# Performance work log

Measured on AMD Instinct MI355X. Metric: run time of the kernel, lower is better.

Reference implementation:

```python
import jax, jax.numpy as jnp
import numpy as np

RADIUS = 4  # matches init radius


def _bilinear_sample(v, grid):
    """Faithful F.grid_sample(v, grid, mode='bilinear', align_corners=True, padding_mode='zeros').
    v: (B,C,H,W); grid: (B,Hg,Wg,2) in [-1,1]; grid[...,0]->width(x), grid[...,1]->height(y)."""
    B, C, H, W = v.shape
    Hg, Wg = grid.shape[1], grid.shape[2]
    ix = (grid[..., 0] + 1.0) * 0.5 * (W - 1)
    iy = (grid[..., 1] + 1.0) * 0.5 * (H - 1)
    x0 = jnp.floor(ix); y0 = jnp.floor(iy)
    x1 = x0 + 1.0;      y1 = y0 + 1.0
    wx1 = ix - x0; wx0 = 1.0 - wx1
    wy1 = iy - y0; wy0 = 1.0 - wy1
    v_flat = v.reshape(B, C, H * W)
    out = jnp.zeros((B, C, Hg, Wg), v.dtype)
    for xf, yf, w in ((x0, y0, wx0 * wy0), (x1, y0, wx1 * wy0),
                      (x0, y1, wx0 * wy1), (x1, y1, wx1 * wy1)):
        valid = (xf >= 0) & (xf <= W - 1) & (yf >= 0) & (yf <= H - 1)
        xi = jnp.clip(xf, 0, W - 1).astype(jnp.int32)
        yi = jnp.clip(yf, 0, H - 1).astype(jnp.int32)
        idx = (yi * W + xi).reshape(B, 1, Hg * Wg)
        g = jnp.take_along_axis(v_flat, idx, axis=2).reshape(B, C, Hg, Wg)
        out = out + g * (w * valid)[:, None, :, :]
    return out


def setup_inputs() -> dict:
    key = jax.random.key(0)
    ks = jax.random.split(key, 5)
    B, C, H, W, K = 4, 128, 128, 128, 8
    x = jax.random.normal(ks[0], (B, C, H, W), jnp.float32)
    psf_tbl = jax.random.randint(ks[1], (B, H, W, K, 2), 0, 128)  # absolute pixel anchors
    delta = jax.random.normal(ks[2], (1, 1, 1, K, 2), jnp.float32) * 0.1
    w_qkv = jax.random.normal(ks[3], (3 * C, C), jnp.float32) * (C ** -0.5)  # 1x1 conv, no bias
    w_proj = jax.random.normal(ks[4], (C, C), jnp.float32) * (C ** -0.5)
    return {"x": x, "psf_tbl": psf_tbl, "delta": delta, "w_qkv": w_qkv, "w_proj": w_proj}


def reference(x, psf_tbl, delta, w_qkv, w_proj):
    B, C, H, W = x.shape
    K = psf_tbl.shape[3]
    qkv = jnp.einsum('oc,bchw->bohw', w_qkv, x)  # 1x1 conv to_qkv
    q, k, v = jnp.split(qkv, 3, axis=1)
    offsets = psf_tbl.astype(x.dtype) + jnp.tanh(delta) * RADIUS  # (B,H,W,K,2)
    norm = jnp.array([H - 1, W - 1], x.dtype)
    grid = (offsets / norm * 2.0 - 1.0).reshape(B, H, W * K, 2)
    k_s = _bilinear_sample(k, grid).reshape(B, C, H, W, K)
    v_s = _bilinear_sample(v, grid).reshape(B, C, H, W, K)
    attn = jnp.einsum('bchw,bchwk->bhwk', q, k_s) * (C ** -0.5)
    attn = jax.nn.softmax(attn, axis=-1)  # softmax over K sampled points
    out = jnp.einsum('bhwk,bchwk->bchw', attn, v_s)
    return x + jnp.einsum('oc,bchw->bohw', w_proj, out)
```

## Files before the change

kernel.cpp:

```cpp
#include <hip/hip_runtime.h>

#define HW 16384
#define C 128

typedef __attribute__((ext_vector_type(8))) short short8;
typedef __attribute__((ext_vector_type(4))) float f32x4;
typedef __attribute__((ext_vector_type(2))) float f32x2;

__device__ __forceinline__ unsigned short f2bf(float f) {
  union { float f; unsigned u; } v; v.f = f;
  return (unsigned short)((v.u + 0x7fffu + ((v.u >> 16) & 1u)) >> 16);
}
#if __has_builtin(__builtin_amdgcn_cvt_pk_bf16_f32)
typedef __attribute__((ext_vector_type(2))) __bf16 bf16x2;
__device__ __forceinline__ unsigned pk2(float a, float b) {
  union { bf16x2 v; unsigned u; } cv;
  cv.v = __builtin_amdgcn_cvt_pk_bf16_f32(a, b);
  return cv.u;
}
#else
__device__ __forceinline__ unsigned pk2(float a, float b) {
  return (unsigned)f2bf(a) | ((unsigned)f2bf(b) << 16);
}
#endif
__device__ __forceinline__ unsigned short f2bf1(float a) {
  return (unsigned short)(pk2(a, a) & 0xffffu);
}
__device__ __forceinline__ float bflo(unsigned w) {
  union { unsigned u; float f; } v; v.u = w << 16; return v.f;
}
__device__ __forceinline__ float bfhi(unsigned w) {
  union { unsigned u; float f; } v; v.u = w & 0xffff0000u; return v.f;
}
__device__ __forceinline__ float asf(unsigned u) {
  union { unsigned u; float f; } v; v.u = u; return v.f;
}

__global__ __launch_bounds__(128) void k_prep(const float* __restrict__ w_qkv,
                                              const float* __restrict__ w_proj,
                                              const float* __restrict__ delta,
                                              unsigned short* __restrict__ Mt,
                                              unsigned short* __restrict__ Pm,
                                              float* __restrict__ pw,
                                              int* __restrict__ pi) {
  const int bid = blockIdx.x;
  const int t = threadIdx.x;
  if (bid == 256) {
    if (t < 8) {
      float s0 = tanhf(delta[t * 2 + 0]) * 4.0f;
      float s1 = tanhf(delta[t * 2 + 1]) * 4.0f;
      float f0 = floorf(s0), f1 = floorf(s1);
      pi[2 * t + 0] = (int)f0;
      pi[2 * t + 1] = (int)f1;
      float fx = s0 - f0, fy = s1 - f1;
      pw[4 * t + 0] = (1.0f - fx) * (1.0f - fy);
      pw[4 * t + 1] = fx * (1.0f - fy);
      pw[4 * t + 2] = (1.0f - fx) * fy;
      pw[4 * t + 3] = fx * fy;
    }
    return;
  }
  const int R = bid & 127;
  float acc = 0.0f;
  if (bid < 128) {
    const float* wq = w_qkv;
    const float* wk = w_qkv + 128 * 128;
    #pragma unroll 16
    for (int j = 0; j < 128; ++j)
      acc += wk[j * 128 + R] * wq[j * 128 + t];
    acc *= 0.08838834764831845f;
    Mt[R * 128 + (t ^ ((R & 7) << 3))] = f2bf1(acc);
  } else {
    const float* wv = w_qkv + 2 * 128 * 128;
    const float* wp = w_proj + (size_t)R * 128;
    #pragma unroll 16
    for (int j = 0; j < 128; ++j)
      acc += wp[j] * wv[j * 128 + t];
    Pm[R * 128 + (t ^ ((R & 7) << 3))] = f2bf1(acc);
  }
}

__global__ __launch_bounds__(256) void k_qx(const float* __restrict__ x,
                                            const unsigned short* __restrict__ Mt,
                                            unsigned short* __restrict__ qb,
                                            unsigned* __restrict__ xq) {
  __shared__ __align__(16) unsigned char smem[65536];
  unsigned short* Xs = (unsigned short*)smem;
  unsigned short* Ws = (unsigned short*)(smem + 32768);
  const int t = threadIdx.x;
  const int gpix0 = blockIdx.x * 128;
  const int b = gpix0 >> 14;
  const int hw0 = gpix0 & (HW - 1);

  const float* xb = x + (size_t)b * C * HW + hw0;
  #pragma unroll
  for (int i = 0; i < 16; ++i) {
    int linear = i * 256 + t;
    int p = linear & 127;
    int c4 = (linear >> 7) * 4;
    float a0 = xb[(size_t)(c4 + 0) * HW + p];
    float a1 = xb[(size_t)(c4 + 1) * HW + p];
    float a2 = xb[(size_t)(c4 + 2) * HW + p];
    float a3 = xb[(size_t)(c4 + 3) * HW + p];
    int cc = c4 ^ ((p & 7) << 3);
    *(uint2*)&Xs[p * 128 + cc] = make_uint2(pk2(a0, a1), pk2(a2, a3));
  }
  #pragma unroll
  for (int i = 0; i < 8; ++i)
    ((uint4*)Ws)[i * 256 + t] = ((const uint4*)Mt)[i * 256 + t];
  __syncthreads();

  #pragma unroll
  for (int i = 0; i < 8; ++i) {
    int linear = i * 256 + t;
    int c8 = (linear & 15) * 8;
    int prow = linear >> 4;
    uint4 v = *(const uint4*)&Xs[prow * 128 + (c8 ^ ((prow & 7) << 3))];
    *(uint4*)&xq[((size_t)(gpix0 + prow)) * 64 + (c8 >> 1)] = v;
  }

  const int wave = t >> 6, lane = t & 63;
  const int wr = wave >> 1, wc = wave & 1;
  const int rsel = lane & 15, quad = lane >> 4;

  f32x4 acc[4][4];
  #pragma unroll
  for (int mi = 0; mi < 4; ++mi)
    #pragma unroll
    for (int ni = 0; ni < 4; ++ni) acc[mi][ni] = (f32x4){0.f, 0.f, 0.f, 0.f};
  #pragma unroll
  for (int ks = 0; ks < 4; ++ks) {
    const int koff = ks * 32 + quad * 8;
    short8 afr[4], bfr[4];
    #pragma unroll
    for (int mi = 0; mi < 4; ++mi) {
      int r = wr * 64 + mi * 16 + rsel;
      afr[mi] = *(const short8*)&Xs[r * 128 + (koff ^ ((r & 7) << 3))];
    }
    #pragma unroll
    for (int ni = 0; ni < 4; ++ni) {
      int r = wc * 64 + ni * 16 + rsel;
      bfr[ni] = *(const short8*)&Ws[r * 128 + (koff ^ ((r & 7) << 3))];
    }
    #pragma unroll
    for (int mi = 0; mi < 4; ++mi)
      #pragma unroll
      for (int ni = 0; ni < 4; ++ni)
        acc[mi][ni] = __builtin_amdgcn_mfma_f32_16x16x32_bf16(afr[mi], bfr[ni], acc[mi][ni], 0, 0, 0);
  }
  #pragma unroll
  for (int mi = 0; mi < 4; ++mi)
    #pragma unroll
    for (int ni = 0; ni < 4; ++ni)
      #pragma unroll
      for (int r = 0; r < 4; ++r) {
        int pix = gpix0 + wr * 64 + mi * 16 + quad * 4 + r;
        int ch = wc * 64 + ni * 16 + rsel;
        qb[(size_t)pix * C + ch] = f2bf1(acc[mi][ni][r]);
      }
}

__global__ __launch_bounds__(256) void k_attn(const unsigned short* __restrict__ qb,
                                              const unsigned* __restrict__ xq,
                                              const int* __restrict__ psf,
                                              const unsigned* __restrict__ pwu,
                                              const int* __restrict__ pi,
                                              unsigned short* __restrict__ ao) {
  const int t = threadIdx.x;
  const int lane = t & 63;
  const int p = blockIdx.x;
  const int b = (p >> 1) & 3;
  const int j = ((p >> 3) << 1) | (p & 1);
  const int spix = __builtin_amdgcn_readfirstlane((b << 14) + (j << 2) + (t >> 6));

  const unsigned* xB = xq + (size_t)b * HW * 64;

  const unsigned qp = ((const unsigned*)qb)[(size_t)spix * 64 + lane];
  const float qx = bflo(qp), qy = bfhi(qp);

  int anch[16];
  #pragma unroll
  for (int jj = 0; jj < 16; ++jj)
    anch[jj] = __builtin_amdgcn_readfirstlane(psf[(size_t)spix * 16 + jj]);
  int pis[16];
  #pragma unroll
  for (int jj = 0; jj < 16; ++jj)
    pis[jj] = __builtin_amdgcn_readfirstlane(pi[jj]);
  unsigned pws[32];
  #pragma unroll
  for (int jj = 0; jj < 32; ++jj)
    pws[jj] = __builtin_amdgcn_readfirstlane(pwu[jj]);

  float dk[8];
  float2 xt[8];
  #pragma unroll
  for (int k = 0; k < 8; ++k) {
    const int x0 = anch[k * 2 + 0] + pis[2 * k + 0];
    const int y0 = anch[k * 2 + 1] + pis[2 * k + 1];
    float sx = 0.f, sy = 0.f;
    #pragma unroll
    for (int cn = 0; cn < 4; ++cn) {
      const int xi = x0 + (cn & 1);
      const int yi = y0 + (cn >> 1);
      const bool valid = (xi >= 0) & (xi <= 127) & (yi >= 0) & (yi <= 127);
      const int xc = min(max(xi, 0), 127);
      const int yc = min(max(yi, 0), 127);
      const unsigned wb = valid ? pws[k * 4 + cn] : 0u;
      const float wv = asf(wb);
      const unsigned w = xB[((size_t)((yc << 7) + xc) << 6) + lane];
      sx = fmaf(bflo(w), wv, sx);
      sy = fmaf(bfhi(w), wv, sy);
    }
    xt[k] = make_float2(sx, sy);
    dk[k] = fmaf(qx, sx, qy * sy);
  }
  #pragma unroll
  for (int off = 32; off > 0; off >>= 1) {
    #pragma unroll
    for (int k = 0; k < 8; ++k) dk[k] += __shfl_xor(dk[k], off);
  }
  float m = dk[0];
  #pragma unroll
  for (int k = 1; k < 8; ++k) m = fmaxf(m, dk[k]);
  float e[8], den = 0.0f;
  #pragma unroll
  for (int k = 0; k < 8; ++k) { e[k] = __expf(dk[k] - m); den += e[k]; }
  const float inv = 1.0f / den;
  float ox = 0, oy = 0;
  #pragma unroll
  for (int k = 0; k < 8; ++k) { float pk = e[k] * inv; ox += pk * xt[k].x; oy += pk * xt[k].y; }
  ((unsigned*)ao)[(size_t)spix * 64 + lane] = pk2(ox, oy);
}

__global__ __launch_bounds__(256) void k_proj(const unsigned short* __restrict__ ao,
                                              const unsigned short* __restrict__ Pm,
                                              const float* __restrict__ x,
                                              float* __restrict__ out) {
  __shared__ __align__(16) unsigned short As[128 * 128];
  __shared__ __align__(16) unsigned short Ws[128 * 128];
  const int t = threadIdx.x;
  const int gpix0 = blockIdx.x * 128;
  const int b = gpix0 >> 14;
  const int hw0 = gpix0 & (HW - 1);

  #pragma unroll
  for (int i = 0; i < 8; ++i) {
    int linear = i * 256 + t;
    int c8 = (linear & 15) * 8;
    int p = linear >> 4;
    uint4 v = *(const uint4*)(ao + (size_t)(gpix0 + p) * C + c8);
    *(uint4*)&As[p * 128 + (c8 ^ ((p & 7) << 3))] = v;
  }
  #pragma unroll
  for (int i = 0; i < 8; ++i)
    ((uint4*)Ws)[i * 256 + t] = ((const uint4*)Pm)[i * 256 + t];
  __syncthreads();

  const int wave = t >> 6, lane = t & 63;
  const int wr = wave >> 1, wc = wave & 1;
  const int rsel = lane & 15, quad = lane >> 4;

  f32x4 acc[4][4];
  #pragma unroll
  for (int mi = 0; mi < 4; ++mi)
    #pragma unroll
    for (int ni = 0; ni < 4; ++ni) acc[mi][ni] = (f32x4){0.f, 0.f, 0.f, 0.f};

  #pragma unroll
  for (int ks = 0; ks < 4; ++ks) {
    const int koff = ks * 32 + quad * 8;
    short8 afr[4], bfr[4];
    #pragma unroll
    for (int mi = 0; mi < 4; ++mi) {
      int r = wr * 64 + mi * 16 + rsel;
      afr[mi] = *(const short8*)&Ws[r * 128 + (koff ^ ((r & 7) << 3))];
    }
    #pragma unroll
    for (int ni = 0; ni < 4; ++ni) {
      int r = wc * 64 + ni * 16 + rsel;
      bfr[ni] = *(const short8*)&As[r * 128 + (koff ^ ((r & 7) << 3))];
    }
    #pragma unroll
    for (int mi = 0; mi < 4; ++mi)
      #pragma unroll
      for (int ni = 0; ni < 4; ++ni)
        acc[mi][ni] = __builtin_amdgcn_mfma_f32_16x16x32_bf16(afr[mi], bfr[ni], acc[mi][ni], 0, 0, 0);
  }

  #pragma unroll
  for (int mi = 0; mi < 4; ++mi)
    #pragma unroll
    for (int ni = 0; ni < 4; ++ni)
      #pragma unroll
      for (int r = 0; r < 4; ++r) {
        int och = wr * 64 + mi * 16 + quad * 4 + r;
        int pixl = wc * 64 + ni * 16 + rsel;
        size_t addr = ((size_t)b * C + och) * HW + hw0 + pixl;
        out[addr] = x[addr] + acc[mi][ni][r];
      }
}

extern "C" void kernel_launch(void* const* d_in, const int* in_sizes, int n_in,
                              void* d_out, int out_size, void* d_ws, size_t ws_size,
                              hipStream_t stream) {
  const float* x      = (const float*)d_in[0];
  const int*   psf    = (const int*)d_in[1];
  const float* delta  = (const float*)d_in[2];
  const float* w_qkv  = (const float*)d_in[3];
  const float* w_proj = (const float*)d_in[4];
  float* out = (float*)d_out;

  const size_t N = (size_t)4 * HW * C;
  unsigned short* qb = (unsigned short*)d_ws;
  unsigned short* xq = qb + N;
  unsigned short* ao = xq + N;
  unsigned short* Mt = ao + N;
  unsigned short* Pm = Mt + 16384;
  float* pw = (float*)(Pm + 16384);
  int*   pi = (int*)(pw + 32);

  k_prep<<<dim3(257), 128, 0, stream>>>(w_qkv, w_proj, delta, Mt, Pm, pw, pi);
  k_qx<<<dim3(512), 256, 0, stream>>>(x, Mt, qb, (unsigned*)xq);
  k_attn<<<dim3(HW), 256, 0, stream>>>(qb, (const unsigned*)xq, psf, (const unsigned*)pw, pi, ao);
  k_proj<<<dim3(512), 256, 0, stream>>>(ao, Pm, x, out);
}
```

Measured before the change: 154.8 us.

## Shrink GEMM tiles, read weights from global, batch scalar loads in attention

The qkv and projection GEMM kernels now handle 64 pixels per block instead of 128, doubling the grid and halving LDS so more blocks can be resident. Weight tiles are no longer staged in LDS and are read directly from global memory. The q output is restaged through LDS for coalesced 16-byte stores. In the attention kernel, the per-pixel anchors and the shared weight/offset tables are fetched with a few wide scalar loads in inline asm instead of many readfirstlane loads. The trade-off is that fragments read from global memory inside the MFMA loop may add latency, and the inline asm relies on the fixed layout of the workspace.

Result: slower. 163.0 us (+5.3%).

```diff
diff --git a/kernel.cpp b/kernel.cpp
--- a/kernel.cpp
+++ b/kernel.cpp
@@ -6,6 +6,7 @@
 typedef __attribute__((ext_vector_type(8))) short short8;
 typedef __attribute__((ext_vector_type(4))) float f32x4;
 typedef __attribute__((ext_vector_type(2))) float f32x2;
+typedef __attribute__((ext_vector_type(16))) int v16i;
 
 __device__ __forceinline__ unsigned short f2bf(float f) {
   union { float f; unsigned u; } v; v.f = f;
@@ -32,8 +33,8 @@
 __device__ __forceinline__ float bfhi(unsigned w) {
   union { unsigned u; float f; } v; v.u = w & 0xffff0000u; return v.f;
 }
-__device__ __forceinline__ float asf(unsigned u) {
-  union { unsigned u; float f; } v; v.u = u; return v.f;
+__device__ __forceinline__ float asf(int u) {
+  union { int u; float f; } v; v.u = u; return v.f;
 }
 
 __global__ __launch_bounds__(128) void k_prep(const float* __restrict__ w_qkv,
@@ -84,20 +85,18 @@
                                             const unsigned short* __restrict__ Mt,
                                             unsigned short* __restrict__ qb,
                                             unsigned* __restrict__ xq) {
-  __shared__ __align__(16) unsigned char smem[65536];
-  unsigned short* Xs = (unsigned short*)smem;
-  unsigned short* Ws = (unsigned short*)(smem + 32768);
+  __shared__ __align__(16) unsigned short Xs[64 * 128];
   const int t = threadIdx.x;
-  const int gpix0 = blockIdx.x * 128;
+  const int gpix0 = blockIdx.x * 64;
   const int b = gpix0 >> 14;
   const int hw0 = gpix0 & (HW - 1);
 
   const float* xb = x + (size_t)b * C * HW + hw0;
   #pragma unroll
-  for (int i = 0; i < 16; ++i) {
+  for (int i = 0; i < 8; ++i) {
     int linear = i * 256 + t;
-    int p = linear & 127;
-    int c4 = (linear >> 7) * 4;
+    int p = linear & 63;
+    int c4 = (linear >> 6) * 4;
     float a0 = xb[(size_t)(c4 + 0) * HW + p];
     float a1 = xb[(size_t)(c4 + 1) * HW + p];
     float a2 = xb[(size_t)(c4 + 2) * HW + p];
@@ -105,13 +104,10 @@
     int cc = c4 ^ ((p & 7) << 3);
     *(uint2*)&Xs[p * 128 + cc] = make_uint2(pk2(a0, a1), pk2(a2, a3));
   }
-  #pragma unroll
-  for (int i = 0; i < 8; ++i)
-    ((uint4*)Ws)[i * 256 + t] = ((const uint4*)Mt)[i * 256 + t];
   __syncthreads();
 
   #pragma unroll
-  for (int i = 0; i < 8; ++i) {
+  for (int i = 0; i < 4; ++i) {
     int linear = i * 256 + t;
     int c8 = (linear & 15) * 8;
     int prow = linear >> 4;
@@ -123,49 +119,60 @@
   const int wr = wave >> 1, wc = wave & 1;
   const int rsel = lane & 15, quad = lane >> 4;
 
-  f32x4 acc[4][4];
-  #pragma unroll
-  for (int mi = 0; mi < 4; ++mi)
+  f32x4 acc[2][4];
+  #pragma unroll
+  for (int mi = 0; mi < 2; ++mi)
     #pragma unroll
     for (int ni = 0; ni < 4; ++ni) acc[mi][ni] = (f32x4){0.f, 0.f, 0.f, 0.f};
   #pragma unroll
   for (int ks = 0; ks < 4; ++ks) {
     const int koff = ks * 32 + quad * 8;
-    short8 afr[4], bfr[4];
-    #pragma unroll
-    for (int mi = 0; mi < 4; ++mi) {
-      int r = wr * 64 + mi * 16 + rsel;
+    short8 afr[2], bfr[4];
+    #pragma unroll
+    for (int mi = 0; mi < 2; ++mi) {
+      int r = wr * 32 + mi * 16 + rsel;
       afr[mi] = *(const short8*)&Xs[r * 128 + (koff ^ ((r & 7) << 3))];
     }
     #pragma unroll
     for (int ni = 0; ni < 4; ++ni) {
       int r = wc * 64 + ni * 16 + rsel;
-      bfr[ni] = *(const short8*)&Ws[r * 128 + (koff ^ ((r & 7) << 3))];
-    }
-    #pragma unroll
-    for (int mi = 0; mi < 4; ++mi)
+      bfr[ni] = *(const short8*)&Mt[r * 128 + (koff ^ ((r & 7) << 3))];
+    }
+    #pragma unroll
+    for (int mi = 0; mi < 2; ++mi)
       #pragma unroll
       for (int ni = 0; ni < 4; ++ni)
         acc[mi][ni] = __builtin_amdgcn_mfma_f32_16x16x32_bf16(afr[mi], bfr[ni], acc[mi][ni], 0, 0, 0);
   }
-  #pragma unroll
-  for (int mi = 0; mi < 4; ++mi)
+  __syncthreads();
+  #pragma unroll
+  for (int mi = 0; mi < 2; ++mi)
     #pragma unroll
     for (int ni = 0; ni < 4; ++ni)
       #pragma unroll
       for (int r = 0; r < 4; ++r) {
-        int pix = gpix0 + wr * 64 + mi * 16 + quad * 4 + r;
+        int p = wr * 32 + mi * 16 + quad * 4 + r;
         int ch = wc * 64 + ni * 16 + rsel;
-        qb[(size_t)pix * C + ch] = f2bf1(acc[mi][ni][r]);
+        Xs[p * 128 + (ch ^ ((p & 7) << 3))] = f2bf1(acc[mi][ni][r]);
       }
+  __syncthreads();
+  #pragma unroll
+  for (int i = 0; i < 4; ++i) {
+    int linear = i * 256 + t;
+    int c8 = (linear & 15) * 8;
+    int prow = linear >> 4;
+    uint4 v = *(const uint4*)&Xs[prow * 128 + (c8 ^ ((prow & 7) << 3))];
+    *(uint4*)(qb + (size_t)(gpix0 + prow) * C + c8) = v;
+  }
 }
 
 __global__ __launch_bounds__(256) void k_attn(const unsigned short* __restrict__ qb,
                                               const unsigned* __restrict__ xq,
                                               const int* __restrict__ psf,
-                                              const unsigned* __restrict__ pwu,
+                                              const int* __restrict__ pwu,
                                               const int* __restrict__ pi,
                                               unsigned short* __restrict__ ao) {
+  (void)pi;
   const int t = threadIdx.x;
   const int lane = t & 63;
   const int p = blockIdx.x;
@@ -178,25 +185,22 @@
   const unsigned qp = ((const unsigned*)qb)[(size_t)spix * 64 + lane];
   const float qx = bflo(qp), qy = bfhi(qp);
 
-  int anch[16];
-  #pragma unroll
-  for (int jj = 0; jj < 16; ++jj)
-    anch[jj] = __builtin_amdgcn_readfirstlane(psf[(size_t)spix * 16 + jj]);
-  int pis[16];
-  #pragma unroll
-  for (int jj = 0; jj < 16; ++jj)
-    pis[jj] = __builtin_amdgcn_readfirstlane(pi[jj]);
-  unsigned pws[32];
-  #pragma unroll
-  for (int jj = 0; jj < 32; ++jj)
-    pws[jj] = __builtin_amdgcn_readfirstlane(pwu[jj]);
+  v16i w0, w1, tpi, ps;
+  asm volatile(
+      "s_load_dwordx16 %0, %4, 0\n\t"
+      "s_load_dwordx16 %1, %4, 64\n\t"
+      "s_load_dwordx16 %2, %4, 128\n\t"
+      "s_load_dwordx16 %3, %5, 0\n\t"
+      "s_waitcnt lgkmcnt(0)"
+      : "=&s"(w0), "=&s"(w1), "=&s"(tpi), "=&s"(ps)
+      : "s"(pwu), "s"(psf + (size_t)spix * 16));
 
   float dk[8];
   float2 xt[8];
   #pragma unroll
   for (int k = 0; k < 8; ++k) {
-    const int x0 = anch[k * 2 + 0] + pis[2 * k + 0];
-    const int y0 = anch[k * 2 + 1] + pis[2 * k + 1];
+    const int x0 = ps[k * 2 + 0] + tpi[2 * k + 0];
+    const int y0 = ps[k * 2 + 1] + tpi[2 * k + 1];
     float sx = 0.f, sy = 0.f;
     #pragma unroll
     for (int cn = 0; cn < 4; ++cn) {
@@ -205,8 +209,9 @@
       const bool valid = (xi >= 0) & (xi <= 127) & (yi >= 0) & (yi <= 127);
       const int xc = min(max(xi, 0), 127);
       const int yc = min(max(yi, 0), 127);
-      const unsigned wb = valid ? pws[k * 4 + cn] : 0u;
-      const float wv = asf(wb);
+      const int widx = k * 4 + cn;
+      const int wbits = (widx < 16) ? w0[widx & 15] : w1[widx & 15];
+      const float wv = asf(valid ? wbits : 0);
       const unsigned w = xB[((size_t)((yc << 7) + xc) << 6) + lane];
       sx = fmaf(bflo(w), wv, sx);
       sy = fmaf(bfhi(w), wv, sy);
@@ -236,65 +241,61 @@
                                               const unsigned short* __restrict__ Pm,
                                               const float* __restrict__ x,
                                               float* __restrict__ out) {
-  __shared__ __align__(16) unsigned short As[128 * 128];
-  __shared__ __align__(16) unsigned short Ws[128 * 128];
+  __shared__ __align__(16) unsigned short As[64 * 128];
   const int t = threadIdx.x;
-  const int gpix0 = blockIdx.x * 128;
+  const int gpix0 = blockIdx.x * 64;
   const int b = gpix0 >> 14;
   const int hw0 = gpix0 & (HW - 1);
 
   #pragma unroll
-  for (int i = 0; i < 8; ++i) {
+  for (int i = 0; i < 4; ++i) {
     int linear = i * 256 + t;
     int c8 = (linear & 15) * 8;
     int p = linear >> 4;
     uint4 v = *(const uint4*)(ao + (size_t)(gpix0 + p) * C + c8);
     *(uint4*)&As[p * 128 + (c8 ^ ((p & 7) << 3))] = v;
   }
-  #pragma unroll
-  for (int i = 0; i < 8; ++i)
-    ((uint4*)Ws)[i * 256 + t] = ((const uint4*)Pm)[i * 256 + t];
   __syncthreads();
 
   const int wave = t >> 6, lane = t & 63;
   const int wr = wave >> 1, wc = wave & 1;
   const int rsel = lane & 15, quad = lane >> 4;
 
-  f32x4 acc[4][4];
+  f32x4 acc[4][2];
   #pragma unroll
   for (int mi = 0; mi < 4; ++mi)
     #pragma unroll
-    for (int ni = 0; ni < 4; ++ni) acc[mi][ni] = (f32x4){0.f, 0.f, 0.f, 0.f};
+    for (int ni = 0; ni < 2; ++ni) acc[mi][ni] = (f32x4){0.f, 0.f, 0.f, 0.f};
 
   #pragma unroll
   for (int ks = 0; ks < 4; ++ks) {
     const int koff = ks * 32 + quad * 8;
-    short8 afr[4], bfr[4];
+    short8 afr[4], bfr[2];
     #pragma unroll
     for (int mi = 0; mi < 4; ++mi) {
       int r = wr * 64 + mi * 16 + rsel;
-      afr[mi] = *(const short8*)&Ws[r * 128 + (koff ^ ((r & 7) << 3))];
-    }
-    #pragma unroll
-    for (int ni = 0; ni < 4; ++ni) {
-      int r = wc * 64 + ni * 16 + rsel;
+      afr[mi] = *(const short8*)&Pm[r * 128 + (koff ^ ((r & 7) << 3))];
+    }
+    #pragma unroll
+    for (int ni = 0; ni < 2; ++ni) {
+      int r = wc * 32 + ni * 16 + rsel;
       bfr[ni] = *(const short8*)&As[r * 128 + (koff ^ ((r & 7) << 3))];
     }
     #pragma unroll
     for (int mi = 0; mi < 4; ++mi)
       #pragma unroll
-      for (int ni = 0; ni < 4; ++ni)
+      for (int ni = 0; ni < 2; ++ni)
         acc[mi][ni] = __builtin_amdgcn_mfma_f32_16x16x32_bf16(afr[mi], bfr[ni], acc[mi][ni], 0, 0, 0);
   }
 
   #pragma unroll
   for (int mi = 0; mi < 4; ++mi)
     #pragma unroll
-    for (int ni = 0; ni < 4; ++ni)
+    for (int ni = 0; ni < 2; ++ni)
       #pragma unroll
       for (int r = 0; r < 4; ++r) {
         int och = wr * 64 + mi * 16 + quad * 4 + r;
-        int pixl = wc * 64 + ni * 16 + rsel;
+        int pixl = wc * 32 + ni * 16 + rsel;
         size_t addr = ((size_t)b * C + och) * HW + hw0 + pixl;
         out[addr] = x[addr] + acc[mi][ni][r];
       }
@@ -320,7 +321,7 @@
   int*   pi = (int*)(pw + 32);
 
   k_prep<<<dim3(257), 128, 0, stream>>>(w_qkv, w_proj, delta, Mt, Pm, pw, pi);
-  k_qx<<<dim3(512), 256, 0, stream>>>(x, Mt, qb, (unsigned*)xq);
-  k_attn<<<dim3(HW), 256, 0, stream>>>(qb, (const unsigned*)xq, psf, (const unsigned*)pw, pi, ao);
-  k_proj<<<dim3(512), 256, 0, stream>>>(ao, Pm, x, out);
-}
+  k_qx<<<dim3(1024), 256, 0, stream>>>(x, Mt, qb, (unsigned*)xq);
+  k_attn<<<dim3(HW), 256, 0, stream>>>(qb, (const unsigned*)xq, psf, (const int*)pw, pi, ao);
+  k_proj<<<dim3(1024), 256, 0, stream>>>(ao, Pm, x, out);
+}
```

## Coalesce q stores via LDS, batch scalar loads in attn, reuse bf16 x residual

Applied to the files above, without the earlier changes.

k_qx now stages its q output tile through shared memory and writes it back in 16-byte coalesced rows, replacing scattered 2-byte global stores. k_attn replaces the per-element readfirstlane loads with inline-asm s_load_dwordx16 batches for the weights, integer offsets and anchors, and issues all 32 gathers before the arithmetic so their latency overlaps. k_proj reads the residual from the existing bf16 copy of x through LDS instead of the fp32 input, halving residual traffic. The residual shortcut adds bf16 rounding error to the output. The inline asm assumes pi sits directly after pw in the workspace.

New measurement: 154.1 us. Within noise of the previous version (-0.4%).

```diff
diff --git a/kernel.cpp b/kernel.cpp
--- a/kernel.cpp
+++ b/kernel.cpp
@@ -6,6 +6,7 @@
 typedef __attribute__((ext_vector_type(8))) short short8;
 typedef __attribute__((ext_vector_type(4))) float f32x4;
 typedef __attribute__((ext_vector_type(2))) float f32x2;
+typedef __attribute__((ext_vector_type(16))) int v16i;
 
 __device__ __forceinline__ unsigned short f2bf(float f) {
   union { float f; unsigned u; } v; v.f = f;
@@ -32,8 +33,11 @@
 __device__ __forceinline__ float bfhi(unsigned w) {
   union { unsigned u; float f; } v; v.u = w & 0xffff0000u; return v.f;
 }
-__device__ __forceinline__ float asf(unsigned u) {
-  union { unsigned u; float f; } v; v.u = u; return v.f;
+__device__ __forceinline__ float asf(int u) {
+  union { int u; float f; } v; v.u = u; return v.f;
+}
+__device__ __forceinline__ float bf2f(unsigned short h) {
+  union { unsigned u; float f; } v; v.u = ((unsigned)h) << 16; return v.f;
 }
 
 __global__ __launch_bounds__(128) void k_prep(const float* __restrict__ w_qkv,
@@ -148,24 +152,35 @@
       for (int ni = 0; ni < 4; ++ni)
         acc[mi][ni] = __builtin_amdgcn_mfma_f32_16x16x32_bf16(afr[mi], bfr[ni], acc[mi][ni], 0, 0, 0);
   }
+  __syncthreads();
   #pragma unroll
   for (int mi = 0; mi < 4; ++mi)
     #pragma unroll
     for (int ni = 0; ni < 4; ++ni)
       #pragma unroll
       for (int r = 0; r < 4; ++r) {
-        int pix = gpix0 + wr * 64 + mi * 16 + quad * 4 + r;
+        int p = wr * 64 + mi * 16 + quad * 4 + r;
         int ch = wc * 64 + ni * 16 + rsel;
-        qb[(size_t)pix * C + ch] = f2bf1(acc[mi][ni][r]);
+        Xs[p * 128 + (ch ^ ((p & 7) << 3))] = f2bf1(acc[mi][ni][r]);
       }
+  __syncthreads();
+  #pragma unroll
+  for (int i = 0; i < 8; ++i) {
+    int linear = i * 256 + t;
+    int c8 = (linear & 15) * 8;
+    int prow = linear >> 4;
+    uint4 v = *(const uint4*)&Xs[prow * 128 + (c8 ^ ((prow & 7) << 3))];
+    *(uint4*)(qb + (size_t)(gpix0 + prow) * C + c8) = v;
+  }
 }
 
 __global__ __launch_bounds__(256) void k_attn(const unsigned short* __restrict__ qb,
                                               const unsigned* __restrict__ xq,
                                               const int* __restrict__ psf,
-                                              const unsigned* __restrict__ pwu,
+                                              const int* __restrict__ pwu,
                                               const int* __restrict__ pi,
                                               unsigned short* __restrict__ ao) {
+  (void)pi;
   const int t = threadIdx.x;
   const int lane = t & 63;
   const int p = blockIdx.x;
@@ -178,36 +193,45 @@
   const unsigned qp = ((const unsigned*)qb)[(size_t)spix * 64 + lane];
   const float qx = bflo(qp), qy = bfhi(qp);
 
-  int anch[16];
-  #pragma unroll
-  for (int jj = 0; jj < 16; ++jj)
-    anch[jj] = __builtin_amdgcn_readfirstlane(psf[(size_t)spix * 16 + jj]);
-  int pis[16];
-  #pragma unroll
-  for (int jj = 0; jj < 16; ++jj)
-    pis[jj] = __builtin_amdgcn_readfirstlane(pi[jj]);
-  unsigned pws[32];
-  #pragma unroll
-  for (int jj = 0; jj < 32; ++jj)
-    pws[jj] = __builtin_amdgcn_readfirstlane(pwu[jj]);
+  v16i w0, w1, tpi, ps;
+  asm volatile(
+      "s_load_dwordx16 %0, %4, 0\n\t"
+      "s_load_dwordx16 %1, %4, 64\n\t"
+      "s_load_dwordx16 %2, %4, 128\n\t"
+      "s_load_dwordx16 %3, %5, 0\n\t"
+      "s_waitcnt lgkmcnt(0)"
+      : "=&s"(w0), "=&s"(w1), "=&s"(tpi), "=&s"(ps)
+      : "s"(pwu), "s"(psf + (size_t)spix * 16));
+
+  unsigned wreg[32];
+  #pragma unroll
+  for (int k = 0; k < 8; ++k) {
+    const int x0 = ps[k * 2 + 0] + tpi[2 * k + 0];
+    const int y0 = ps[k * 2 + 1] + tpi[2 * k + 1];
+    #pragma unroll
+    for (int cn = 0; cn < 4; ++cn) {
+      const int xc = min(max(x0 + (cn & 1), 0), 127);
+      const int yc = min(max(y0 + (cn >> 1), 0), 127);
+      wreg[k * 4 + cn] = xB[((size_t)((yc << 7) + xc) << 6) + lane];
+    }
+  }
 
   float dk[8];
   float2 xt[8];
   #pragma unroll
   for (int k = 0; k < 8; ++k) {
-    const int x0 = anch[k * 2 + 0] + pis[2 * k + 0];
-    const int y0 = anch[k * 2 + 1] + pis[2 * k + 1];
+    const int x0 = ps[k * 2 + 0] + tpi[2 * k + 0];
+    const int y0 = ps[k * 2 + 1] + tpi[2 * k + 1];
     float sx = 0.f, sy = 0.f;
     #pragma unroll
     for (int cn = 0; cn < 4; ++cn) {
       const int xi = x0 + (cn & 1);
       const int yi = y0 + (cn >> 1);
       const bool valid = (xi >= 0) & (xi <= 127) & (yi >= 0) & (yi <= 127);
-      const int xc = min(max(xi, 0), 127);
-      const int yc = min(max(yi, 0), 127);
-      const unsigned wb = valid ? pws[k * 4 + cn] : 0u;
-      const float wv = asf(wb);
-      const unsigned w = xB[((size_t)((yc << 7) + xc) << 6) + lane];
+      const int widx = k * 4 + cn;
+      const int wbits = (widx < 16) ? w0[widx & 15] : w1[widx & 15];
+      const float wv = asf(valid ? wbits : 0);
+      const unsigned w = wreg[widx];
       sx = fmaf(bflo(w), wv, sx);
       sy = fmaf(bfhi(w), wv, sy);
     }
@@ -222,19 +246,19 @@
   float m = dk[0];
   #pragma unroll
   for (int k = 1; k < 8; ++k) m = fmaxf(m, dk[k]);
-  float e[8], den = 0.0f;
-  #pragma unroll
-  for (int k = 0; k < 8; ++k) { e[k] = __expf(dk[k] - m); den += e[k]; }
+  float den = 0.0f;
+  #pragma unroll
+  for (int k = 0; k < 8; ++k) { dk[k] = __expf(dk[k] - m); den += dk[k]; }
   const float inv = 1.0f / den;
   float ox = 0, oy = 0;
   #pragma unroll
-  for (int k = 0; k < 8; ++k) { float pk = e[k] * inv; ox += pk * xt[k].x; oy += pk * xt[k].y; }
+  for (int k = 0; k < 8; ++k) { float pk = dk[k] * inv; ox += pk * xt[k].x; oy += pk * xt[k].y; }
   ((unsigned*)ao)[(size_t)spix * 64 + lane] = pk2(ox, oy);
 }
 
 __global__ __launch_bounds__(256) void k_proj(const unsigned short* __restrict__ ao,
                                               const unsigned short* __restrict__ Pm,
-                                              const float* __restrict__ x,
+                                              const unsigned short* __restrict__ xqh,
                                               float* __restrict__ out) {
   __shared__ __align__(16) unsigned short As[128 * 128];
   __shared__ __align__(16) unsigned short Ws[128 * 128];
@@ -287,6 +311,17 @@
         acc[mi][ni] = __builtin_amdgcn_mfma_f32_16x16x32_bf16(afr[mi], bfr[ni], acc[mi][ni], 0, 0, 0);
   }
 
+  __syncthreads();
+  #pragma unroll
+  for (int i = 0; i < 8; ++i) {
+    int linear = i * 256 + t;
+    int c8 = (linear & 15) * 8;
+    int p = linear >> 4;
+    uint4 v = *(const uint4*)(xqh + (size_t)(gpix0 + p) * C + c8);
+    *(uint4*)&As[p * 128 + (c8 ^ ((p & 7) << 3))] = v;
+  }
+  __syncthreads();
+
   #pragma unroll
   for (int mi = 0; mi < 4; ++mi)
     #pragma unroll
@@ -295,8 +330,9 @@
       for (int r = 0; r < 4; ++r) {
         int och = wr * 64 + mi * 16 + quad * 4 + r;
         int pixl = wc * 64 + ni * 16 + rsel;
+        float xr = bf2f(As[pixl * 128 + (och ^ ((pixl & 7) << 3))]);
         size_t addr = ((size_t)b * C + och) * HW + hw0 + pixl;
-        out[addr] = x[addr] + acc[mi][ni][r];
+        out[addr] = xr + acc[mi][ni][r];
       }
 }
 
@@ -321,6 +357,6 @@
 
   k_prep<<<dim3(257), 128, 0, stream>>>(w_qkv, w_proj, delta, Mt, Pm, pw, pi);
   k_qx<<<dim3(512), 256, 0, stream>>>(x, Mt, qb, (unsigned*)xq);
-  k_attn<<<dim3(HW), 256, 0, stream>>>(qb, (const unsigned*)xq, psf, (const unsigned*)pw, pi, ao);
-  k_proj<<<dim3(512), 256, 0, stream>>>(ao, Pm, x, out);
-}
+  k_attn<<<dim3(HW), 256, 0, stream>>>(qb, (const unsigned*)xq, psf, (const int*)pw, pi, ao);
+  k_proj<<<dim3(512), 256, 0, stream>>>(ao, Pm, xq, out);
+}
```
